# Performance work log

Measured on AMD Instinct MI355X. Metric: run time of the kernel, lower is better.

Reference implementation:

```python
import jax, jax.numpy as jnp
import numpy as np
from jax import lax

B, S, H = 2, 1024, 1024   # batch, seq, hidden_size
I = 512                   # moe_intermediate_size
E = 16                    # num_experts
TOP_K = 8                 # num_experts_per_tok


def setup_inputs() -> dict:
    key = jax.random.key(0)
    ks = jax.random.split(key, 5)
    scale_h = 1.0 / np.sqrt(H)
    scale_i = 1.0 / np.sqrt(I)
    return {
        "hidden_states": jax.random.normal(ks[0], (B, S, H), dtype=jnp.float32),
        "gate_w": jax.random.normal(ks[1], (H, E), dtype=jnp.float32) * scale_h,   # router
        "w_gate": jax.random.normal(ks[2], (E, H, I), dtype=jnp.float32) * scale_h,
        "w_up":   jax.random.normal(ks[3], (E, H, I), dtype=jnp.float32) * scale_h,
        "w_down": jax.random.normal(ks[4], (E, I, H), dtype=jnp.float32) * scale_i,
    }


def reference(hidden_states, gate_w, w_gate, w_up, w_down):
    b, s, h = hidden_states.shape
    x = hidden_states.reshape(-1, h)                      # [T, H]
    T = x.shape[0]

    router_logits = x @ gate_w                            # [T, E]
    probs = jax.nn.softmax(router_logits.astype(jnp.float32), axis=-1)
    top_w, top_i = lax.top_k(probs, TOP_K)                # [T, K]
    top_w = top_w / jnp.sum(top_w, axis=-1, keepdims=True)  # norm_topk_prob
    top_w = top_w.astype(x.dtype)

    # Dense per-token combine weights [T, E]; zero for unselected experts
    combine = jnp.zeros((T, E), dtype=x.dtype)
    combine = combine.at[jnp.arange(T)[:, None], top_i].add(top_w)

    # Scan over experts: masked gated-MLP, weighted accumulate (exact math;
    # unselected tokens contribute with weight 0, matching index_add scatter).
    def expert_step(acc, ws):
        wg, wu, wd, ce = ws                               # ce: [T] combine weights
        hmid = jax.nn.silu(x @ wg) * (x @ wu)             # [T, I]
        return acc + (hmid @ wd) * ce[:, None], None

    out, _ = lax.scan(expert_step, jnp.zeros_like(x),
                      (w_gate, w_up, w_down, combine.T))
    return out.reshape(b, s, h), router_logits
```

## Files before the change

kernel.cpp:

```cpp
#include <hip/hip_runtime.h>

typedef __attribute__((ext_vector_type(8))) short bf16x8;
typedef __attribute__((ext_vector_type(4))) float f32x4;
typedef __attribute__((ext_vector_type(4))) unsigned short u16x4;


static __device__ __forceinline__ unsigned short f2bfu(float f) {
  union { float f; unsigned u; } v; v.f = f;
  return (unsigned short)((v.u + 0x7fffu + ((v.u >> 16) & 1u)) >> 16);
}

static __device__ __forceinline__ float bfu2f(unsigned short u) {
  union { unsigned u; float f; } v; v.u = ((unsigned)u) << 16; return v.f;
}

static __device__ __forceinline__ void gload_lds16(const void* g, void* l) {
  __builtin_amdgcn_global_load_lds(
      (const __attribute__((address_space(1))) unsigned int*)g,
      (__attribute__((address_space(3))) unsigned int*)l, 16, 0, 0);
}

__global__ __launch_bounds__(256) void k_transall(const float* __restrict__ wga,
                                                  const float* __restrict__ wup,
                                                  const float* __restrict__ wdo,
                                                  unsigned short* __restrict__ wgt,
                                                  unsigned short* __restrict__ wut,
                                                  unsigned short* __restrict__ wdt2) {
  __shared__ float tile[64][65];
  const int z = blockIdx.z;
  const float* src;
  unsigned short* dst;
  int R, C, ostride;
  if (z < 16)      { src = wga + (size_t)z * 524288; dst = wgt + (size_t)z * 524288; R = 1024; C = 512; ostride = 1024; }
  else if (z < 32) { src = wup + (size_t)(z-16) * 524288; dst = wut + (size_t)(z-16) * 524288; R = 1024; C = 512; ostride = 1024; }
  else             { src = wdo + (size_t)(z-32) * 524288; dst = wdt2 + (size_t)(z-32) * 524288; R = 512; C = 1024; ostride = 512; }
  int c0 = blockIdx.x * 64, r0 = blockIdx.y * 64;
  if (c0 >= C || r0 >= R) return;
  int cc = (threadIdx.x & 15) * 4, rr = threadIdx.x >> 4;
#pragma unroll
  for (int i = 0; i < 4; ++i) {
    float4 v = *(const float4*)(src + (size_t)(r0 + rr + i * 16) * C + c0 + cc);
    tile[rr + i * 16][cc + 0] = v.x; tile[rr + i * 16][cc + 1] = v.y;
    tile[rr + i * 16][cc + 2] = v.z; tile[rr + i * 16][cc + 3] = v.w;
  }
  __syncthreads();
#pragma unroll
  for (int i = 0; i < 4; ++i) {
    int oc = rr + i * 16;
    u16x4 o = { f2bfu(tile[cc + 0][oc]), f2bfu(tile[cc + 1][oc]),
                f2bfu(tile[cc + 2][oc]), f2bfu(tile[cc + 3][oc]) };
    *(u16x4*)(dst + (size_t)(c0 + oc) * ostride + r0 + cc) = o;
  }
}

__global__ __launch_bounds__(64) void k_router(const float* __restrict__ x,
                                               const float* __restrict__ gw,
                                               float* __restrict__ combine,
                                               float* __restrict__ logits,
                                               unsigned short* __restrict__ xb) {
  int t = blockIdx.x;
  int lane = threadIdx.x;
  const float* xr = x + (size_t)t * 1024;
  unsigned short* xbr = xb + (size_t)t * 1024;
  float acc[16];
#pragma unroll
  for (int e = 0; e < 16; ++e) acc[e] = 0.f;
  for (int h = lane; h < 1024; h += 64) {
    float xv = xr[h];
    xbr[h] = f2bfu(xv);
    const float4* gr = (const float4*)(gw + (size_t)h * 16);
#pragma unroll
    for (int q = 0; q < 4; ++q) {
      float4 g4 = gr[q];
      acc[q * 4 + 0] += xv * g4.x;
      acc[q * 4 + 1] += xv * g4.y;
      acc[q * 4 + 2] += xv * g4.z;
      acc[q * 4 + 3] += xv * g4.w;
    }
  }
#pragma unroll
  for (int e = 0; e < 16; ++e) {
#pragma unroll
    for (int off = 32; off > 0; off >>= 1)
      acc[e] += __shfl_xor(acc[e], off);
  }
  if (lane < 16) logits[(size_t)t * 16 + lane] = acc[lane];

  float m = acc[0];
#pragma unroll
  for (int e = 1; e < 16; ++e) m = fmaxf(m, acc[e]);
  unsigned sel = 0u;
  for (int k = 0; k < 8; ++k) {
    float best = -3.4e38f; int bi = 0;
#pragma unroll
    for (int e = 0; e < 16; ++e)
      if (!((sel >> e) & 1u) && acc[e] > best) { best = acc[e]; bi = e; }
    sel |= 1u << bi;
  }
  float s = 0.f;
#pragma unroll
  for (int e = 0; e < 16; ++e)
    if ((sel >> e) & 1u) s += expf(acc[e] - m);
  float inv = 1.f / s;
  if (lane < 16)
    combine[(size_t)t * 16 + lane] = ((sel >> lane) & 1u) ? expf(acc[lane] - m) * inv : 0.f;
}

__global__ __launch_bounds__(256) void k_scan(const float* __restrict__ combine,
                                              unsigned short* __restrict__ idxlist,
                                              int* __restrict__ tokslot,
                                              int* __restrict__ counts) {
  __shared__ int wsum[4];
  const int e = blockIdx.x;
  const int tid = threadIdx.x;
  const int lane = tid & 63, w = tid >> 6;
  const int t0 = tid * 8;
  int flags = 0, cnt = 0;
#pragma unroll
  for (int j = 0; j < 8; ++j) {
    float c = combine[(size_t)(t0 + j) * 16 + e];
    if (c != 0.f) { flags |= 1 << j; ++cnt; }
  }
  int scan = cnt;
#pragma unroll
  for (int off = 1; off < 64; off <<= 1) {
    int v = __shfl_up(scan, off);
    if (lane >= off) scan += v;
  }
  if (lane == 63) wsum[w] = scan;
  __syncthreads();
  int base = 0;
  for (int i = 0; i < w; ++i) base += wsum[i];
  int pos = base + scan - cnt;
  for (int j = 0; j < 8; ++j) {
    if ((flags >> j) & 1) {
      idxlist[e * 2048 + pos] = (unsigned short)(t0 + j);
      tokslot[(t0 + j) * 16 + e] = pos;
      ++pos;
    } else {
      tokslot[(t0 + j) * 16 + e] = -1;
    }
  }
  if (tid == 255) counts[e] = base + scan;
}

__global__ __launch_bounds__(64) void k_offsets(const int* __restrict__ counts,
                                                int* __restrict__ ebase,
                                                int* __restrict__ pairs,
                                                int* __restrict__ pM) {
  int lane = threadIdx.x;
  int c = (lane < 16) ? counts[lane] : 0;
  int s = c;
#pragma unroll
  for (int off = 1; off < 16; off <<= 1) {
    int v = __shfl_up(s, off);
    if (lane >= off) s += v;
  }
  if (lane < 16) ebase[lane] = s - c;
  int nt = (lane < 16) ? ((c + 127) >> 7) : 0;
  int ts = nt;
#pragma unroll
  for (int off = 1; off < 16; off <<= 1) {
    int v = __shfl_up(ts, off);
    if (lane >= off) ts += v;
  }
  if (lane < 16) {
    int tb = ts - nt;
    for (int j = 0; j < nt; ++j) pairs[tb + j] = (lane << 4) | j;
  }
  if (lane == 15) pM[0] = ts;
}

__global__ __launch_bounds__(256) void k_gateup(const unsigned short* __restrict__ xb,
                                                const unsigned short* __restrict__ wgt,
                                                const unsigned short* __restrict__ wut,
                                                const unsigned short* __restrict__ idxlist,
                                                const int* __restrict__ counts,
                                                const int* __restrict__ ebase,
                                                const int* __restrict__ pairs,
                                                const int* __restrict__ pM,
                                                unsigned short* __restrict__ midp) {
  const int lb = (int)(blockIdx.x & 7) * 256 + (int)(blockIdx.x >> 3);
  const int p = lb & 255, it = lb >> 8;
  if (p >= pM[0]) return;
  const int e = pairs[p] >> 4, mt = pairs[p] & 15;
  const int Ne = counts[e];
  const int m0 = mt * 128;
  const int i0 = it * 64;

  __shared__ alignas(16) char lds[32768];

  const int tid = threadIdx.x;
  const int lane = tid & 63;
  const int w = tid >> 6;
  const int wm = (w >> 1) * 64;
  const int wn = (w & 1) * 32;
  const int gb = ebase[e];

  const int crow = lane >> 2;
  const int slog = (lane & 3) ^ ((crow >> 1) & 3);

  const unsigned short* wge = wgt + (size_t)e * (512 * 1024);
  const unsigned short* wue = wut + (size_t)e * (512 * 1024);

  const unsigned short* gsrc[4];
  int loff[4];
#pragma unroll
  for (int q = 0; q < 4; ++q) {
    int c = w * 4 + q;
    loff[q] = c * 1024;
    if (c < 8) {
      int slot = m0 + c * 16 + crow;
      slot = slot < Ne ? slot : Ne - 1;
      gsrc[q] = xb + (size_t)idxlist[e * 2048 + slot] * 1024 + slog * 8;
    } else if (c < 12) {
      gsrc[q] = wge + (size_t)(i0 + (c - 8) * 16 + crow) * 1024 + slog * 8;
    } else {
      gsrc[q] = wue + (size_t)(i0 + (c - 12) * 16 + crow) * 1024 + slog * 8;
    }
  }

  auto stage = [&](int buf, int k0) {
    char* base = lds + buf * 16384;
#pragma unroll
    for (int q = 0; q < 4; ++q)
      gload_lds16(gsrc[q] + k0, base + loff[q]);
  };

  const int r0 = lane & 15;
  const int gp16 = ((lane >> 4) ^ ((r0 >> 1) & 3)) << 4;
  const int aoff  = ((wm + r0) << 6) + gp16;
  const int bgoff = 8192  + ((wn + r0) << 6) + gp16;
  const int buoff = 12288 + ((wn + r0) << 6) + gp16;

  f32x4 accg[4][2], accu[4][2];
#pragma unroll
  for (int fm = 0; fm < 4; ++fm)
#pragma unroll
    for (int fn = 0; fn < 2; ++fn) {
      accg[fm][fn] = f32x4{0.f, 0.f, 0.f, 0.f};
      accu[fm][fn] = f32x4{0.f, 0.f, 0.f, 0.f};
    }

  stage(0, 0);
  stage(1, 32);
  for (int t = 0; t < 32; ++t) {
    const int cur = t & 1;
    if (t == 31) asm volatile("s_waitcnt vmcnt(0)" ::: "memory");
    else         asm volatile("s_waitcnt vmcnt(4)" ::: "memory");
    __builtin_amdgcn_s_barrier();
    const char* base = lds + cur * 16384;
    bf16x8 a[4], bg[2], bu[2];
#pragma unroll
    for (int fm = 0; fm < 4; ++fm) a[fm] = *(const bf16x8*)(base + aoff + fm * 1024);
#pragma unroll
    for (int fn = 0; fn < 2; ++fn) {
      bg[fn] = *(const bf16x8*)(base + bgoff + fn * 1024);
      bu[fn] = *(const bf16x8*)(base + buoff + fn * 1024);
    }
    asm volatile("s_waitcnt lgkmcnt(0)" ::: "memory");
    __builtin_amdgcn_sched_barrier(0);
    __builtin_amdgcn_s_barrier();
    if (t + 2 < 32) stage(cur, (t + 2) * 32);
    __builtin_amdgcn_s_setprio(1);
#pragma unroll
    for (int fm = 0; fm < 4; ++fm)
#pragma unroll
      for (int fn = 0; fn < 2; ++fn) {
        accg[fm][fn] = __builtin_amdgcn_mfma_f32_16x16x32_bf16(a[fm], bg[fn], accg[fm][fn], 0, 0, 0);
        accu[fm][fn] = __builtin_amdgcn_mfma_f32_16x16x32_bf16(a[fm], bu[fn], accu[fm][fn], 0, 0, 0);
      }
    __builtin_amdgcn_s_setprio(0);
  }

  const int gq = lane >> 4;
#pragma unroll
  for (int fm = 0; fm < 4; ++fm) {
#pragma unroll
    for (int jj = 0; jj < 4; ++jj) {
      int slot = m0 + wm + fm * 16 + gq * 4 + jj;
      if (slot >= Ne) continue;
#pragma unroll
      for (int fn = 0; fn < 2; ++fn) {
        float gv = accg[fm][fn][jj];
        float uv = accu[fm][fn][jj];
        float mv = gv / (1.f + __expf(-gv)) * uv;
        midp[(size_t)(gb + slot) * 512 + i0 + wn + fn * 16 + r0] = f2bfu(mv);
      }
    }
  }
}

__global__ __launch_bounds__(256) void k_down(const unsigned short* __restrict__ midp,
                                              const unsigned short* __restrict__ wdt2,
                                              const int* __restrict__ counts,
                                              const int* __restrict__ ebase,
                                              const int* __restrict__ pairs,
                                              const int* __restrict__ pM,
                                              unsigned short* __restrict__ dpk) {
  const int lb = (int)(blockIdx.x & 7) * 512 + (int)(blockIdx.x >> 3);
  const int p = lb & 255, ht = lb >> 8;
  if (p >= pM[0]) return;
  const int e = pairs[p] >> 4, mt = pairs[p] & 15;
  const int Ne = counts[e];
  const int m0 = mt * 128;
  const int h0 = ht * 64;

  __shared__ alignas(16) char lds[24576];

  const int tid = threadIdx.x;
  const int lane = tid & 63;
  const int w = tid >> 6;
  const int wm = (w >> 1) * 64;
  const int wn = (w & 1) * 32;
  const int gb = ebase[e];

  const int crow = lane >> 2;
  const int slog = (lane & 3) ^ ((crow >> 1) & 3);

  const unsigned short* bsrc = wdt2 + (size_t)e * (512 * 1024);

  const unsigned short* gsrc[3];
  int loff[3];
#pragma unroll
  for (int q = 0; q < 3; ++q) {
    int c = w * 3 + q;
    loff[q] = c * 1024;
    if (c < 8) {
      int slot = m0 + c * 16 + crow;
      slot = slot < Ne ? slot : Ne - 1;
      gsrc[q] = midp + (size_t)(gb + slot) * 512 + slog * 8;
    } else {
      gsrc[q] = bsrc + (size_t)(h0 + (c - 8) * 16 + crow) * 512 + slog * 8;
    }
  }

  auto stage = [&](int buf, int k0) {
    char* base = lds + buf * 12288;
#pragma unroll
    for (int q = 0; q < 3; ++q)
      gload_lds16(gsrc[q] + k0, base + loff[q]);
  };

  const int r0 = lane & 15;
  const int gp16 = ((lane >> 4) ^ ((r0 >> 1) & 3)) << 4;
  const int aoff = ((wm + r0) << 6) + gp16;
  const int boff = 8192 + ((wn + r0) << 6) + gp16;

  f32x4 acc[4][2];
#pragma unroll
  for (int fm = 0; fm < 4; ++fm)
#pragma unroll
    for (int fn = 0; fn < 2; ++fn) acc[fm][fn] = f32x4{0.f, 0.f, 0.f, 0.f};

  stage(0, 0);
  stage(1, 32);
  for (int t = 0; t < 16; ++t) {
    const int cur = t & 1;
    if (t == 15) asm volatile("s_waitcnt vmcnt(0)" ::: "memory");
    else         asm volatile("s_waitcnt vmcnt(3)" ::: "memory");
    __builtin_amdgcn_s_barrier();
    const char* base = lds + cur * 12288;
    bf16x8 a[4], b[2];
#pragma unroll
    for (int fm = 0; fm < 4; ++fm) a[fm] = *(const bf16x8*)(base + aoff + fm * 1024);
#pragma unroll
    for (int fn = 0; fn < 2; ++fn) b[fn] = *(const bf16x8*)(base + boff + fn * 1024);
    asm volatile("s_waitcnt lgkmcnt(0)" ::: "memory");
    __builtin_amdgcn_sched_barrier(0);
    __builtin_amdgcn_s_barrier();
    if (t + 2 < 16) stage(cur, (t + 2) * 32);
    __builtin_amdgcn_s_setprio(1);
#pragma unroll
    for (int fm = 0; fm < 4; ++fm)
#pragma unroll
      for (int fn = 0; fn < 2; ++fn)
        acc[fm][fn] = __builtin_amdgcn_mfma_f32_16x16x32_bf16(a[fm], b[fn], acc[fm][fn], 0, 0, 0);
    __builtin_amdgcn_s_setprio(0);
  }

  const int gq = lane >> 4;
#pragma unroll
  for (int fm = 0; fm < 4; ++fm)
#pragma unroll
    for (int jj = 0; jj < 4; ++jj) {
      int slot = m0 + wm + fm * 16 + gq * 4 + jj;
      if (slot >= Ne) continue;
#pragma unroll
      for (int fn = 0; fn < 2; ++fn)
        dpk[(size_t)(gb + slot) * 1024 + h0 + wn + fn * 16 + r0] = f2bfu(acc[fm][fn][jj]);
    }
}

__global__ __launch_bounds__(128) void k_combine(const unsigned short* __restrict__ dpk,
                                                 const int* __restrict__ tokslot,
                                                 const int* __restrict__ ebase,
                                                 const float* __restrict__ combine,
                                                 float* __restrict__ out) {
  __shared__ int gsl[16];
  __shared__ float cws[16];
  const int t = blockIdx.x;
  const int tid = threadIdx.x;
  if (tid < 16) {
    int sl = tokslot[t * 16 + tid];
    gsl[tid] = (sl >= 0) ? ebase[tid] + sl : -1;
    cws[tid] = combine[(size_t)t * 16 + tid];
  }
  __syncthreads();
  float av[8];
#pragma unroll
  for (int j = 0; j < 8; ++j) av[j] = 0.f;
#pragma unroll
  for (int e = 0; e < 16; ++e) {
    int g = gsl[e];
    if (g < 0) continue;
    float cw = cws[e];
    bf16x8 v = *(const bf16x8*)(dpk + (size_t)g * 1024 + tid * 8);
#pragma unroll
    for (int j = 0; j < 8; ++j) av[j] += cw * bfu2f((unsigned short)v[j]);
  }
  float4 lo = { av[0], av[1], av[2], av[3] };
  float4 hi = { av[4], av[5], av[6], av[7] };
  float4* op = (float4*)(out + (size_t)t * 1024 + tid * 8);
  op[0] = lo;
  op[1] = hi;
}

extern "C" void kernel_launch(void* const* d_in, const int* in_sizes, int n_in,
                              void* d_out, int out_size, void* d_ws, size_t ws_size,
                              hipStream_t stream) {
  const float* x   = (const float*)d_in[0];
  const float* gw  = (const float*)d_in[1];
  const float* wga = (const float*)d_in[2];
  const float* wup = (const float*)d_in[3];
  const float* wdo = (const float*)d_in[4];
  float* out = (float*)d_out;
  float* logits = out + (size_t)2048 * 1024;

  char* ws = (char*)d_ws;
  unsigned short* xb   = (unsigned short*)(ws + 0);
  unsigned short* wgt  = (unsigned short*)(ws + 4194304);
  unsigned short* wut  = (unsigned short*)(ws + 20971520);
  unsigned short* wdt2 = (unsigned short*)(ws + 37748736);
  unsigned short* midp = (unsigned short*)(ws + 54525952);
  float* combine       = (float*)(ws + 71303168);
  int* tokslot         = (int*)(ws + 71434240);
  unsigned short* idxl = (unsigned short*)(ws + 71565312);
  int* counts          = (int*)(ws + 71630848);
  int* ebase           = (int*)(ws + 71630912);
  int* pairs           = (int*)(ws + 71630976);
  int* pM              = (int*)(ws + 71632000);
  unsigned short* dpk  = (unsigned short*)(ws + 4194304);

  k_transall<<<dim3(16, 16, 48), 256, 0, stream>>>(wga, wup, wdo, wgt, wut, wdt2);
  k_router<<<2048, 64, 0, stream>>>(x, gw, combine, logits, xb);
  k_scan<<<16, 256, 0, stream>>>(combine, idxl, tokslot, counts);
  k_offsets<<<1, 64, 0, stream>>>(counts, ebase, pairs, pM);
  k_gateup<<<2048, 256, 0, stream>>>(xb, wgt, wut, idxl, counts, ebase, pairs, pM, midp);
  k_down<<<4096, 256, 0, stream>>>(midp, wdt2, counts, ebase, pairs, pM, dpk);
  k_combine<<<2048, 128, 0, stream>>>(dpk, tokslot, ebase, combine, out);
}
```

Baseline: 159.0 us.

## Deepen gate/up K-tile and widen down-proj M-tile to 256 rows

In the gate/up kernel, each pipeline stage now covers a 64-wide K-slice instead of 32. It uses a 64 KB double buffer with a new 8-way XOR swizzle, which halves the number of barrier and wait iterations. The down-projection kernel moves to 512 threads with a 256-row M tile per block, so the weight tile loaded from global memory is shared by twice as many rows. Blocks are now indexed directly by expert, M-tile and H-tile, with an early exit for empty tiles, instead of going through the pairs list. The trade-off is more LDS per block and larger, possibly half-empty tiles for experts with few tokens, which may lower occupancy.

```diff
diff --git a/kernel.cpp b/kernel.cpp
--- a/kernel.cpp
+++ b/kernel.cpp
@@ -188,7 +188,7 @@
   const int m0 = mt * 128;
   const int i0 = it * 64;
 
-  __shared__ alignas(16) char lds[32768];
+  __shared__ alignas(16) char lds[65536];
 
   const int tid = threadIdx.x;
   const int lane = tid & 63;
@@ -197,41 +197,54 @@
   const int wn = (w & 1) * 32;
   const int gb = ebase[e];
 
-  const int crow = lane >> 2;
-  const int slog = (lane & 3) ^ ((crow >> 1) & 3);
+  const int srow8 = lane >> 3;
+  const int sls = (lane & 7) ^ (srow8 & 7);
 
   const unsigned short* wge = wgt + (size_t)e * (512 * 1024);
   const unsigned short* wue = wut + (size_t)e * (512 * 1024);
 
-  const unsigned short* gsrc[4];
-  int loff[4];
-#pragma unroll
-  for (int q = 0; q < 4; ++q) {
-    int c = w * 4 + q;
+  const unsigned short* gsrc[8];
+  int loff[8];
+#pragma unroll
+  for (int q = 0; q < 8; ++q) {
+    int c = w * 8 + q;
     loff[q] = c * 1024;
-    if (c < 8) {
-      int slot = m0 + c * 16 + crow;
+    if (c < 16) {
+      int slot = m0 + c * 8 + srow8;
       slot = slot < Ne ? slot : Ne - 1;
-      gsrc[q] = xb + (size_t)idxlist[e * 2048 + slot] * 1024 + slog * 8;
-    } else if (c < 12) {
-      gsrc[q] = wge + (size_t)(i0 + (c - 8) * 16 + crow) * 1024 + slog * 8;
+      gsrc[q] = xb + (size_t)idxlist[e * 2048 + slot] * 1024 + sls * 8;
+    } else if (c < 24) {
+      gsrc[q] = wge + (size_t)(i0 + (c - 16) * 8 + srow8) * 1024 + sls * 8;
     } else {
-      gsrc[q] = wue + (size_t)(i0 + (c - 12) * 16 + crow) * 1024 + slog * 8;
+      gsrc[q] = wue + (size_t)(i0 + (c - 24) * 8 + srow8) * 1024 + sls * 8;
     }
   }
 
   auto stage = [&](int buf, int k0) {
-    char* base = lds + buf * 16384;
-#pragma unroll
-    for (int q = 0; q < 4; ++q)
+    char* base = lds + buf * 32768;
+#pragma unroll
+    for (int q = 0; q < 8; ++q)
       gload_lds16(gsrc[q] + k0, base + loff[q]);
   };
 
   const int r0 = lane & 15;
-  const int gp16 = ((lane >> 4) ^ ((r0 >> 1) & 3)) << 4;
-  const int aoff  = ((wm + r0) << 6) + gp16;
-  const int bgoff = 8192  + ((wn + r0) << 6) + gp16;
-  const int buoff = 12288 + ((wn + r0) << 6) + gp16;
+  const int g4 = lane >> 4;
+  int aoff[4][2], bgoff[2][2], buoff[2][2];
+#pragma unroll
+  for (int ks = 0; ks < 2; ++ks) {
+#pragma unroll
+    for (int fm = 0; fm < 4; ++fm) {
+      int r = wm + fm * 16 + r0;
+      aoff[fm][ks] = (r >> 3) * 1024 + (r & 7) * 128 + (((ks * 4 + g4) ^ (r & 7)) << 4);
+    }
+#pragma unroll
+    for (int fn = 0; fn < 2; ++fn) {
+      int r = wn + fn * 16 + r0;
+      int off = (r >> 3) * 1024 + (r & 7) * 128 + (((ks * 4 + g4) ^ (r & 7)) << 4);
+      bgoff[fn][ks] = 16384 + off;
+      buoff[fn][ks] = 24576 + off;
+    }
+  }
 
   f32x4 accg[4][2], accu[4][2];
 #pragma unroll
@@ -243,42 +256,46 @@
     }
 
   stage(0, 0);
-  stage(1, 32);
-  for (int t = 0; t < 32; ++t) {
+  stage(1, 64);
+  for (int t = 0; t < 16; ++t) {
     const int cur = t & 1;
-    if (t == 31) asm volatile("s_waitcnt vmcnt(0)" ::: "memory");
-    else         asm volatile("s_waitcnt vmcnt(4)" ::: "memory");
+    if (t == 15) asm volatile("s_waitcnt vmcnt(0)" ::: "memory");
+    else         asm volatile("s_waitcnt vmcnt(8)" ::: "memory");
     __builtin_amdgcn_s_barrier();
-    const char* base = lds + cur * 16384;
-    bf16x8 a[4], bg[2], bu[2];
-#pragma unroll
-    for (int fm = 0; fm < 4; ++fm) a[fm] = *(const bf16x8*)(base + aoff + fm * 1024);
-#pragma unroll
-    for (int fn = 0; fn < 2; ++fn) {
-      bg[fn] = *(const bf16x8*)(base + bgoff + fn * 1024);
-      bu[fn] = *(const bf16x8*)(base + buoff + fn * 1024);
+    const char* base = lds + cur * 32768;
+    bf16x8 a[4][2], bg[2][2], bu[2][2];
+#pragma unroll
+    for (int ks = 0; ks < 2; ++ks) {
+#pragma unroll
+      for (int fm = 0; fm < 4; ++fm) a[fm][ks] = *(const bf16x8*)(base + aoff[fm][ks]);
+#pragma unroll
+      for (int fn = 0; fn < 2; ++fn) {
+        bg[fn][ks] = *(const bf16x8*)(base + bgoff[fn][ks]);
+        bu[fn][ks] = *(const bf16x8*)(base + buoff[fn][ks]);
+      }
     }
     asm volatile("s_waitcnt lgkmcnt(0)" ::: "memory");
     __builtin_amdgcn_sched_barrier(0);
     __builtin_amdgcn_s_barrier();
-    if (t + 2 < 32) stage(cur, (t + 2) * 32);
+    if (t + 2 < 16) stage(cur, (t + 2) * 64);
     __builtin_amdgcn_s_setprio(1);
 #pragma unroll
-    for (int fm = 0; fm < 4; ++fm)
-#pragma unroll
-      for (int fn = 0; fn < 2; ++fn) {
-        accg[fm][fn] = __builtin_amdgcn_mfma_f32_16x16x32_bf16(a[fm], bg[fn], accg[fm][fn], 0, 0, 0);
-        accu[fm][fn] = __builtin_amdgcn_mfma_f32_16x16x32_bf16(a[fm], bu[fn], accu[fm][fn], 0, 0, 0);
-      }
+    for (int ks = 0; ks < 2; ++ks)
+#pragma unroll
+      for (int fm = 0; fm < 4; ++fm)
+#pragma unroll
+        for (int fn = 0; fn < 2; ++fn) {
+          accg[fm][fn] = __builtin_amdgcn_mfma_f32_16x16x32_bf16(a[fm][ks], bg[fn][ks], accg[fm][fn], 0, 0, 0);
+          accu[fm][fn] = __builtin_amdgcn_mfma_f32_16x16x32_bf16(a[fm][ks], bu[fn][ks], accu[fm][fn], 0, 0, 0);
+        }
     __builtin_amdgcn_s_setprio(0);
   }
 
-  const int gq = lane >> 4;
 #pragma unroll
   for (int fm = 0; fm < 4; ++fm) {
 #pragma unroll
     for (int jj = 0; jj < 4; ++jj) {
-      int slot = m0 + wm + fm * 16 + gq * 4 + jj;
+      int slot = m0 + wm + fm * 16 + g4 * 4 + jj;
       if (slot >= Ne) continue;
 #pragma unroll
       for (int fn = 0; fn < 2; ++fn) {
@@ -291,22 +308,19 @@
   }
 }
 
-__global__ __launch_bounds__(256) void k_down(const unsigned short* __restrict__ midp,
+__global__ __launch_bounds__(512) void k_down(const unsigned short* __restrict__ midp,
                                               const unsigned short* __restrict__ wdt2,
                                               const int* __restrict__ counts,
                                               const int* __restrict__ ebase,
-                                              const int* __restrict__ pairs,
-                                              const int* __restrict__ pM,
                                               unsigned short* __restrict__ dpk) {
-  const int lb = (int)(blockIdx.x & 7) * 512 + (int)(blockIdx.x >> 3);
-  const int p = lb & 255, ht = lb >> 8;
-  if (p >= pM[0]) return;
-  const int e = pairs[p] >> 4, mt = pairs[p] & 15;
+  const int lb = (int)(blockIdx.x & 7) * 256 + (int)(blockIdx.x >> 3);
+  const int mt = lb & 7, ht = (lb >> 3) & 15, e = lb >> 7;
   const int Ne = counts[e];
-  const int m0 = mt * 128;
+  const int m0 = mt * 256;
+  if (m0 >= Ne) return;
   const int h0 = ht * 64;
 
-  __shared__ alignas(16) char lds[24576];
+  __shared__ alignas(16) char lds[40960];
 
   const int tid = threadIdx.x;
   const int lane = tid & 63;
@@ -320,32 +334,35 @@
 
   const unsigned short* bsrc = wdt2 + (size_t)e * (512 * 1024);
 
-  const unsigned short* gsrc[3];
-  int loff[3];
-#pragma unroll
-  for (int q = 0; q < 3; ++q) {
-    int c = w * 3 + q;
-    loff[q] = c * 1024;
-    if (c < 8) {
-      int slot = m0 + c * 16 + crow;
-      slot = slot < Ne ? slot : Ne - 1;
-      gsrc[q] = midp + (size_t)(gb + slot) * 512 + slog * 8;
-    } else {
-      gsrc[q] = bsrc + (size_t)(h0 + (c - 8) * 16 + crow) * 512 + slog * 8;
-    }
+  const unsigned short* gsrcA[2];
+  int loffA[2];
+#pragma unroll
+  for (int q = 0; q < 2; ++q) {
+    int c = q * 8 + w;
+    loffA[q] = c * 1024;
+    int slot = m0 + c * 16 + crow;
+    slot = slot < Ne ? slot : Ne - 1;
+    gsrcA[q] = midp + (size_t)(gb + slot) * 512 + slog * 8;
+  }
+  const unsigned short* gsrcB = nullptr;
+  int loffB = 0;
+  if (w >= 4) {
+    loffB = 16384 + (w - 4) * 1024;
+    gsrcB = bsrc + (size_t)(h0 + (w - 4) * 16 + crow) * 512 + slog * 8;
   }
 
   auto stage = [&](int buf, int k0) {
-    char* base = lds + buf * 12288;
-#pragma unroll
-    for (int q = 0; q < 3; ++q)
-      gload_lds16(gsrc[q] + k0, base + loff[q]);
+    char* base = lds + buf * 20480;
+#pragma unroll
+    for (int q = 0; q < 2; ++q)
+      gload_lds16(gsrcA[q] + k0, base + loffA[q]);
+    if (gsrcB) gload_lds16(gsrcB + k0, base + loffB);
   };
 
   const int r0 = lane & 15;
   const int gp16 = ((lane >> 4) ^ ((r0 >> 1) & 3)) << 4;
   const int aoff = ((wm + r0) << 6) + gp16;
-  const int boff = 8192 + ((wn + r0) << 6) + gp16;
+  const int boff = 16384 + ((wn + r0) << 6) + gp16;
 
   f32x4 acc[4][2];
 #pragma unroll
@@ -357,10 +374,11 @@
   stage(1, 32);
   for (int t = 0; t < 16; ++t) {
     const int cur = t & 1;
-    if (t == 15) asm volatile("s_waitcnt vmcnt(0)" ::: "memory");
-    else         asm volatile("s_waitcnt vmcnt(3)" ::: "memory");
+    if (t == 15)       asm volatile("s_waitcnt vmcnt(0)" ::: "memory");
+    else if (w >= 4)   asm volatile("s_waitcnt vmcnt(3)" ::: "memory");
+    else               asm volatile("s_waitcnt vmcnt(2)" ::: "memory");
     __builtin_amdgcn_s_barrier();
-    const char* base = lds + cur * 12288;
+    const char* base = lds + cur * 20480;
     bf16x8 a[4], b[2];
 #pragma unroll
     for (int fm = 0; fm < 4; ++fm) a[fm] = *(const bf16x8*)(base + aoff + fm * 1024);
@@ -457,6 +475,6 @@
   k_scan<<<16, 256, 0, stream>>>(combine, idxl, tokslot, counts);
   k_offsets<<<1, 64, 0, stream>>>(counts, ebase, pairs, pM);
   k_gateup<<<2048, 256, 0, stream>>>(xb, wgt, wut, idxl, counts, ebase, pairs, pM, midp);
-  k_down<<<4096, 256, 0, stream>>>(midp, wdt2, counts, ebase, pairs, pM, dpk);
+  k_down<<<2048, 512, 0, stream>>>(midp, wdt2, counts, ebase, dpk);
   k_combine<<<2048, 128, 0, stream>>>(dpk, tokslot, ebase, combine, out);
 }
```

Measured after the change: 150.2 us. 1.06x faster.

## Triple-buffer GEMM staging, drop offsets kernel, enlarge down-proj tiles

Applied to the files above, without the earlier changes.

Removes the k_offsets launch, so each GEMM block now works out its expert, tile and base offset directly from the counts array. Both gate/up and down kernels move from double to triple-buffered LDS staging, which drops the second barrier per k-step. k_down now uses 512-thread blocks with 256-row M tiles and a fixed per-expert grid, which gives more reuse of the weight tile. The trade-offs are higher LDS use that may lower occupancy, and a per-expert grid that launches blocks which exit early.

```diff
diff --git a/kernel.cpp b/kernel.cpp
--- a/kernel.cpp
+++ b/kernel.cpp
@@ -144,58 +144,36 @@
   if (tid == 255) counts[e] = base + scan;
 }
 
-__global__ __launch_bounds__(64) void k_offsets(const int* __restrict__ counts,
-                                                int* __restrict__ ebase,
-                                                int* __restrict__ pairs,
-                                                int* __restrict__ pM) {
-  int lane = threadIdx.x;
-  int c = (lane < 16) ? counts[lane] : 0;
-  int s = c;
-#pragma unroll
-  for (int off = 1; off < 16; off <<= 1) {
-    int v = __shfl_up(s, off);
-    if (lane >= off) s += v;
-  }
-  if (lane < 16) ebase[lane] = s - c;
-  int nt = (lane < 16) ? ((c + 127) >> 7) : 0;
-  int ts = nt;
-#pragma unroll
-  for (int off = 1; off < 16; off <<= 1) {
-    int v = __shfl_up(ts, off);
-    if (lane >= off) ts += v;
-  }
-  if (lane < 16) {
-    int tb = ts - nt;
-    for (int j = 0; j < nt; ++j) pairs[tb + j] = (lane << 4) | j;
-  }
-  if (lane == 15) pM[0] = ts;
-}
-
 __global__ __launch_bounds__(256) void k_gateup(const unsigned short* __restrict__ xb,
                                                 const unsigned short* __restrict__ wgt,
                                                 const unsigned short* __restrict__ wut,
                                                 const unsigned short* __restrict__ idxlist,
                                                 const int* __restrict__ counts,
-                                                const int* __restrict__ ebase,
-                                                const int* __restrict__ pairs,
-                                                const int* __restrict__ pM,
                                                 unsigned short* __restrict__ midp) {
   const int lb = (int)(blockIdx.x & 7) * 256 + (int)(blockIdx.x >> 3);
   const int p = lb & 255, it = lb >> 8;
-  if (p >= pM[0]) return;
-  const int e = pairs[p] >> 4, mt = pairs[p] & 15;
-  const int Ne = counts[e];
+  int e = -1, mt = 0, Ne = 0, gb = 0, acc = 0;
+#pragma unroll
+  for (int i = 0; i < 16; ++i) {
+    int c = counts[i];
+    int nt = (c + 127) >> 7;
+    if (e < 0) {
+      if (p < acc + nt) { e = i; mt = p - acc; Ne = c; }
+      else gb += c;
+    }
+    acc += nt;
+  }
+  if (e < 0) return;
   const int m0 = mt * 128;
   const int i0 = it * 64;
 
-  __shared__ alignas(16) char lds[32768];
+  __shared__ alignas(16) char lds[49152];
 
   const int tid = threadIdx.x;
   const int lane = tid & 63;
   const int w = tid >> 6;
   const int wm = (w >> 1) * 64;
   const int wn = (w & 1) * 32;
-  const int gb = ebase[e];
 
   const int crow = lane >> 2;
   const int slog = (lane & 3) ^ ((crow >> 1) & 3);
@@ -244,8 +222,8 @@
 
   stage(0, 0);
   stage(1, 32);
+  int cur = 0;
   for (int t = 0; t < 32; ++t) {
-    const int cur = t & 1;
     if (t == 31) asm volatile("s_waitcnt vmcnt(0)" ::: "memory");
     else         asm volatile("s_waitcnt vmcnt(4)" ::: "memory");
     __builtin_amdgcn_s_barrier();
@@ -260,8 +238,10 @@
     }
     asm volatile("s_waitcnt lgkmcnt(0)" ::: "memory");
     __builtin_amdgcn_sched_barrier(0);
-    __builtin_amdgcn_s_barrier();
-    if (t + 2 < 32) stage(cur, (t + 2) * 32);
+    if (t + 2 < 32) {
+      int nb = cur + 2; if (nb >= 3) nb -= 3;
+      stage(nb, (t + 2) * 32);
+    }
     __builtin_amdgcn_s_setprio(1);
 #pragma unroll
     for (int fm = 0; fm < 4; ++fm)
@@ -271,6 +251,7 @@
         accu[fm][fn] = __builtin_amdgcn_mfma_f32_16x16x32_bf16(a[fm], bu[fn], accu[fm][fn], 0, 0, 0);
       }
     __builtin_amdgcn_s_setprio(0);
+    if (++cur == 3) cur = 0;
   }
 
   const int gq = lane >> 4;
@@ -291,61 +272,61 @@
   }
 }
 
-__global__ __launch_bounds__(256) void k_down(const unsigned short* __restrict__ midp,
+__global__ __launch_bounds__(512) void k_down(const unsigned short* __restrict__ midp,
                                               const unsigned short* __restrict__ wdt2,
                                               const int* __restrict__ counts,
-                                              const int* __restrict__ ebase,
-                                              const int* __restrict__ pairs,
-                                              const int* __restrict__ pM,
                                               unsigned short* __restrict__ dpk) {
-  const int lb = (int)(blockIdx.x & 7) * 512 + (int)(blockIdx.x >> 3);
-  const int p = lb & 255, ht = lb >> 8;
-  if (p >= pM[0]) return;
-  const int e = pairs[p] >> 4, mt = pairs[p] & 15;
-  const int Ne = counts[e];
-  const int m0 = mt * 128;
+  const int lb = (int)(blockIdx.x & 7) * 256 + (int)(blockIdx.x >> 3);
+  const int mt = lb & 7, ht = (lb >> 3) & 15, e = lb >> 7;
+  int Ne = counts[e], gb = 0;
+#pragma unroll
+  for (int i = 0; i < 16; ++i) { int c = counts[i]; if (i < e) gb += c; }
+  const int m0 = mt * 256;
+  if (m0 >= Ne) return;
   const int h0 = ht * 64;
 
-  __shared__ alignas(16) char lds[24576];
+  __shared__ alignas(16) char lds[61440];
 
   const int tid = threadIdx.x;
   const int lane = tid & 63;
   const int w = tid >> 6;
   const int wm = (w >> 1) * 64;
   const int wn = (w & 1) * 32;
-  const int gb = ebase[e];
 
   const int crow = lane >> 2;
   const int slog = (lane & 3) ^ ((crow >> 1) & 3);
 
   const unsigned short* bsrc = wdt2 + (size_t)e * (512 * 1024);
 
-  const unsigned short* gsrc[3];
-  int loff[3];
-#pragma unroll
-  for (int q = 0; q < 3; ++q) {
-    int c = w * 3 + q;
-    loff[q] = c * 1024;
-    if (c < 8) {
-      int slot = m0 + c * 16 + crow;
-      slot = slot < Ne ? slot : Ne - 1;
-      gsrc[q] = midp + (size_t)(gb + slot) * 512 + slog * 8;
-    } else {
-      gsrc[q] = bsrc + (size_t)(h0 + (c - 8) * 16 + crow) * 512 + slog * 8;
-    }
+  const unsigned short* gsrcA[2];
+  int loffA[2];
+#pragma unroll
+  for (int q = 0; q < 2; ++q) {
+    int c = q * 8 + w;
+    loffA[q] = c * 1024;
+    int slot = m0 + c * 16 + crow;
+    slot = slot < Ne ? slot : Ne - 1;
+    gsrcA[q] = midp + (size_t)(gb + slot) * 512 + slog * 8;
+  }
+  const unsigned short* gsrcB = nullptr;
+  int loffB = 0;
+  if (w >= 4) {
+    loffB = 16384 + (w - 4) * 1024;
+    gsrcB = bsrc + (size_t)(h0 + (w - 4) * 16 + crow) * 512 + slog * 8;
   }
 
   auto stage = [&](int buf, int k0) {
-    char* base = lds + buf * 12288;
-#pragma unroll
-    for (int q = 0; q < 3; ++q)
-      gload_lds16(gsrc[q] + k0, base + loff[q]);
+    char* base = lds + buf * 20480;
+#pragma unroll
+    for (int q = 0; q < 2; ++q)
+      gload_lds16(gsrcA[q] + k0, base + loffA[q]);
+    if (gsrcB) gload_lds16(gsrcB + k0, base + loffB);
   };
 
   const int r0 = lane & 15;
   const int gp16 = ((lane >> 4) ^ ((r0 >> 1) & 3)) << 4;
   const int aoff = ((wm + r0) << 6) + gp16;
-  const int boff = 8192 + ((wn + r0) << 6) + gp16;
+  const int boff = 16384 + ((wn + r0) << 6) + gp16;
 
   f32x4 acc[4][2];
 #pragma unroll
@@ -355,12 +336,13 @@
 
   stage(0, 0);
   stage(1, 32);
+  int cur = 0;
   for (int t = 0; t < 16; ++t) {
-    const int cur = t & 1;
-    if (t == 15) asm volatile("s_waitcnt vmcnt(0)" ::: "memory");
-    else         asm volatile("s_waitcnt vmcnt(3)" ::: "memory");
+    if (t == 15)       asm volatile("s_waitcnt vmcnt(0)" ::: "memory");
+    else if (w >= 4)   asm volatile("s_waitcnt vmcnt(3)" ::: "memory");
+    else               asm volatile("s_waitcnt vmcnt(2)" ::: "memory");
     __builtin_amdgcn_s_barrier();
-    const char* base = lds + cur * 12288;
+    const char* base = lds + cur * 20480;
     bf16x8 a[4], b[2];
 #pragma unroll
     for (int fm = 0; fm < 4; ++fm) a[fm] = *(const bf16x8*)(base + aoff + fm * 1024);
@@ -368,8 +350,10 @@
     for (int fn = 0; fn < 2; ++fn) b[fn] = *(const bf16x8*)(base + boff + fn * 1024);
     asm volatile("s_waitcnt lgkmcnt(0)" ::: "memory");
     __builtin_amdgcn_sched_barrier(0);
-    __builtin_amdgcn_s_barrier();
-    if (t + 2 < 16) stage(cur, (t + 2) * 32);
+    if (t + 2 < 16) {
+      int nb = cur + 2; if (nb >= 3) nb -= 3;
+      stage(nb, (t + 2) * 32);
+    }
     __builtin_amdgcn_s_setprio(1);
 #pragma unroll
     for (int fm = 0; fm < 4; ++fm)
@@ -377,6 +361,7 @@
       for (int fn = 0; fn < 2; ++fn)
         acc[fm][fn] = __builtin_amdgcn_mfma_f32_16x16x32_bf16(a[fm], b[fn], acc[fm][fn], 0, 0, 0);
     __builtin_amdgcn_s_setprio(0);
+    if (++cur == 3) cur = 0;
   }
 
   const int gq = lane >> 4;
@@ -394,7 +379,7 @@
 
 __global__ __launch_bounds__(128) void k_combine(const unsigned short* __restrict__ dpk,
                                                  const int* __restrict__ tokslot,
-                                                 const int* __restrict__ ebase,
+                                                 const int* __restrict__ counts,
                                                  const float* __restrict__ combine,
                                                  float* __restrict__ out) {
   __shared__ int gsl[16];
@@ -402,8 +387,10 @@
   const int t = blockIdx.x;
   const int tid = threadIdx.x;
   if (tid < 16) {
+    int eb = 0;
+    for (int i = 0; i < tid; ++i) eb += counts[i];
     int sl = tokslot[t * 16 + tid];
-    gsl[tid] = (sl >= 0) ? ebase[tid] + sl : -1;
+    gsl[tid] = (sl >= 0) ? eb + sl : -1;
     cws[tid] = combine[(size_t)t * 16 + tid];
   }
   __syncthreads();
@@ -447,16 +434,12 @@
   int* tokslot         = (int*)(ws + 71434240);
   unsigned short* idxl = (unsigned short*)(ws + 71565312);
   int* counts          = (int*)(ws + 71630848);
-  int* ebase           = (int*)(ws + 71630912);
-  int* pairs           = (int*)(ws + 71630976);
-  int* pM              = (int*)(ws + 71632000);
   unsigned short* dpk  = (unsigned short*)(ws + 4194304);
 
   k_transall<<<dim3(16, 16, 48), 256, 0, stream>>>(wga, wup, wdo, wgt, wut, wdt2);
   k_router<<<2048, 64, 0, stream>>>(x, gw, combine, logits, xb);
   k_scan<<<16, 256, 0, stream>>>(combine, idxl, tokslot, counts);
-  k_offsets<<<1, 64, 0, stream>>>(counts, ebase, pairs, pM);
-  k_gateup<<<2048, 256, 0, stream>>>(xb, wgt, wut, idxl, counts, ebase, pairs, pM, midp);
-  k_down<<<4096, 256, 0, stream>>>(midp, wdt2, counts, ebase, pairs, pM, dpk);
-  k_combine<<<2048, 128, 0, stream>>>(dpk, tokslot, ebase, combine, out);
-}
+  k_gateup<<<2048, 256, 0, stream>>>(xb, wgt, wut, idxl, counts, midp);
+  k_down<<<2048, 512, 0, stream>>>(midp, wdt2, counts, dpk);
+  k_combine<<<2048, 128, 0, stream>>>(dpk, tokslot, counts, combine, out);
+}
```

Result: faster. 141.4 us (-11.1%).
